# Kernel optimization log

Measured on AMD Instinct MI355X. Metric: run time of the kernel, lower is better.

## Reference

```python
import jax, jax.numpy as jnp
import numpy as np

B, S, D = 1, 2048, 2048      # batch, seq, hidden
E, F, K = 64, 512, 8         # experts, expert ffn dim, top_k


def setup_inputs() -> dict:
    key = jax.random.key(0)
    ks = jax.random.split(key, 7)
    hidden_states = jax.random.normal(ks[0], (B, S, D), jnp.float32)
    gate_w = jax.random.normal(ks[1], (E, D), jnp.float32) * (D ** -0.5)   # router Linear weight
    w_gate = jax.random.normal(ks[2], (E, F, D), jnp.float32) * 0.02       # expert gate_proj
    w_up   = jax.random.normal(ks[3], (E, F, D), jnp.float32) * 0.02       # expert up_proj
    w_down = jax.random.normal(ks[4], (E, D, F), jnp.float32) * 0.02       # expert down_proj
    token_mod  = jax.random.randint(ks[5], (B * S,), -1, 2).astype(jnp.int32)  # {-1,0,1}
    expert_mod = jax.random.randint(ks[6], (E,), -1, 2).astype(jnp.int32)      # {-1,0,1}
    return {"hidden_states": hidden_states, "gate_w": gate_w, "w_gate": w_gate,
            "w_up": w_up, "w_down": w_down, "token_mod": token_mod,
            "expert_mod": expert_mod}


def reference(hidden_states, gate_w, w_gate, w_up, w_down, token_mod, expert_mod):
    bs = B * S
    x = hidden_states.reshape(bs, D)
    # router gate (Linear, no bias): [bs, E]
    logits = x @ gate_w.T
    # modality pre-filtering: mismatch (tok*exp == -1) -> -inf before softmax
    mismatch = (token_mod[:, None] * expert_mod[None, :]) == -1
    logits = jnp.where(mismatch, -jnp.inf, logits)
    probs = jax.nn.softmax(logits, axis=-1)
    rw, sel = jax.lax.top_k(probs, K)                       # [bs,K]
    rw = rw / jnp.sum(rw, axis=-1, keepdims=True)           # renormalize
    # scatter into sparse routing tensor [bs, E]
    sparse = jnp.zeros((bs, E), x.dtype).at[jnp.arange(bs)[:, None], sel].set(rw)
    # expert dispatch (SwiGLU experts), weighted-sum combine
    g = jnp.einsum('td,efd->tef', x, w_gate)                # [bs,E,F]
    u = jnp.einsum('td,efd->tef', x, w_up)
    h = jax.nn.silu(g) * u
    out = jnp.einsum('te,tef,edf->td', sparse, h, w_down)   # [bs,D]
    return out.reshape(B, S, D)
```

## Files before the change

kernel.cpp:

```cpp
#include <hip/hip_runtime.h>
#include <math.h>

#define BS   2048
#define DIM  2048
#define NE   64
#define NF   512
#define TOPK 8

typedef __attribute__((ext_vector_type(8))) short bf16x8;
typedef __attribute__((ext_vector_type(4))) float f32x4;

__device__ __forceinline__ unsigned cvt2(float lo, float hi) {
    unsigned r;
    asm("v_cvt_pk_bf16_f32 %0, %1, %2" : "=v"(r) : "v"(lo), "v"(hi));
    return r;
}
__device__ __forceinline__ unsigned short f2bf(float f) {
    unsigned r = cvt2(f, 0.f);
    return (unsigned short)(r & 0xFFFF);
}

#define SWZ(r, b) (((((r) << 7) + (b)) ^ (((r) & 7) << 4)))

__global__ __launch_bounds__(256) void zero_kernel(float* __restrict__ out, int* __restrict__ count)
{
    const size_t idx = (size_t)blockIdx.x * blockDim.x + threadIdx.x;
    const size_t tot = (size_t)BS * DIM;
    for (size_t i = idx * 4; i < tot; i += (size_t)gridDim.x * blockDim.x * 4) {
        *(float4*)&out[i] = make_float4(0.f, 0.f, 0.f, 0.f);
    }
    if (idx < NE) count[idx] = 0;
}

__global__ __launch_bounds__(256) void router_kernel(
    const float* __restrict__ x, const float* __restrict__ gate_w,
    const int* __restrict__ token_mod, const int* __restrict__ expert_mod,
    int* __restrict__ count, int* __restrict__ list_token, float* __restrict__ list_w)
{
    __shared__ float xs[4 * DIM];
    __shared__ float pr[4][NE];
    const int t0  = blockIdx.x * 4;
    const int tid = threadIdx.x;
    const int lane = tid & 63, wave = tid >> 6;

    float4* xs4 = (float4*)xs;
    const float4* xr = (const float4*)(x + (size_t)t0 * DIM);
    for (int i = tid; i < 4 * (DIM / 4); i += 256) xs4[i] = xr[i];
    __syncthreads();

    for (int j = 0; j < 16; ++j) {
        const int e = wave * 16 + j;
        const float4* gw = (const float4*)(gate_w + (size_t)e * DIM);
        float s0 = 0.f, s1 = 0.f, s2 = 0.f, s3 = 0.f;
        for (int i = lane; i < DIM / 4; i += 64) {
            const float4 g  = gw[i];
            const float4 v0 = xs4[0 * 512 + i];
            const float4 v1 = xs4[1 * 512 + i];
            const float4 v2 = xs4[2 * 512 + i];
            const float4 v3 = xs4[3 * 512 + i];
            s0 += v0.x * g.x + v0.y * g.y + v0.z * g.z + v0.w * g.w;
            s1 += v1.x * g.x + v1.y * g.y + v1.z * g.z + v1.w * g.w;
            s2 += v2.x * g.x + v2.y * g.y + v2.z * g.z + v2.w * g.w;
            s3 += v3.x * g.x + v3.y * g.y + v3.z * g.z + v3.w * g.w;
        }
        #pragma unroll
        for (int off = 32; off > 0; off >>= 1) {
            s0 += __shfl_xor(s0, off, 64);
            s1 += __shfl_xor(s1, off, 64);
            s2 += __shfl_xor(s2, off, 64);
            s3 += __shfl_xor(s3, off, 64);
        }
        if (lane == 0) {
            pr[0][e] = s0; pr[1][e] = s1; pr[2][e] = s2; pr[3][e] = s3;
        }
    }
    __syncthreads();

    {
        const int t  = t0 + wave;
        const int tm = token_mod[t];
        const int em = expert_mod[lane];
        float p = pr[wave][lane];
        if (tm * em == -1) p = -INFINITY;
        float m0 = p;
        #pragma unroll
        for (int off = 32; off > 0; off >>= 1) m0 = fmaxf(m0, __shfl_xor(m0, off, 64));
        p = __expf(p - m0);
        float s8 = 0.f, wsel = 0.f;
        int   esel = 0;
        #pragma unroll
        for (int k = 0; k < TOPK; ++k) {
            float m = p;
            #pragma unroll
            for (int off = 32; off > 0; off >>= 1) m = fmaxf(m, __shfl_xor(m, off, 64));
            const unsigned long long b = __ballot(p == m);
            const int bi = __ffsll((unsigned long long)b) - 1;
            if (lane == bi) p = -1.f;
            if (lane == k) { esel = bi; wsel = m; }
            s8 += m;
        }
        const float inv = 1.f / s8;
        if (lane < TOPK) {
            const int pos = atomicAdd(&count[esel], 1);
            list_token[esel * BS + pos] = t;
            list_w[esel * BS + pos]     = wsel * inv;
        }
    }
}

__global__ void scan_kernel(const int* __restrict__ count, int* __restrict__ offsets)
{
    if (threadIdx.x == 0) {
        int s = 0;
        for (int e = 0; e < NE; ++e) { offsets[e] = s; s += count[e]; }
    }
}

#define GU_BUF 24576
#define GU_X   0
#define GU_G   8192
#define GU_U   16384

#define GU_COMPUTE(BASE)                                                              \
    {                                                                                 \
        _Pragma("unroll")                                                             \
        for (int ks = 0; ks < 2; ++ks) {                                              \
            const int kb = (ks * 32 + (lane >> 4) * 8) * 2;                           \
            bf16x8 a[2], bg[2], bu[2];                                                \
            _Pragma("unroll")                                                         \
            for (int m = 0; m < 2; ++m)                                               \
                a[m] = *(const bf16x8*)&lds[(BASE) + GU_X + SWZ(wr * 32 + m * 16 + (lane & 15), kb)]; \
            _Pragma("unroll")                                                         \
            for (int nn = 0; nn < 2; ++nn) {                                          \
                const int r = wc * 32 + nn * 16 + (lane & 15);                        \
                bg[nn] = *(const bf16x8*)&lds[(BASE) + GU_G + SWZ(r, kb)];            \
                bu[nn] = *(const bf16x8*)&lds[(BASE) + GU_U + SWZ(r, kb)];            \
            }                                                                         \
            _Pragma("unroll")                                                         \
            for (int m = 0; m < 2; ++m)                                               \
                _Pragma("unroll")                                                     \
                for (int nn = 0; nn < 2; ++nn) {                                      \
                    accg[m][nn] = __builtin_amdgcn_mfma_f32_16x16x32_bf16(a[m], bg[nn], accg[m][nn], 0, 0, 0); \
                    accu[m][nn] = __builtin_amdgcn_mfma_f32_16x16x32_bf16(a[m], bu[nn], accu[m][nn], 0, 0, 0); \
                }                                                                     \
        }                                                                             \
    }

__global__ __launch_bounds__(256, 3) void gateup_mfma(
    const float* __restrict__ x,
    const float* __restrict__ w_gate, const float* __restrict__ w_up,
    const int* __restrict__ count, const int* __restrict__ offsets,
    const int* __restrict__ list_token, const float* __restrict__ list_w,
    unsigned short* __restrict__ h)
{
    const int e  = blockIdx.z;
    const int n  = count[e];
    const int m0 = blockIdx.y * 64;
    if (m0 >= n) return;
    const int f0 = blockIdx.x * 64;
    const int mc = min(64, n - m0);

    __shared__ char  lds[2 * GU_BUF];
    __shared__ int   toks[64];
    __shared__ float rws[64];

    const int tid = threadIdx.x;
    if (tid < 64) {
        const int idx = e * BS + m0 + (tid < mc ? tid : 0);
        toks[tid] = list_token[idx];
        rws[tid]  = (tid < mc) ? list_w[idx] : 0.f;
    }
    __syncthreads();

    const int lane = tid & 63, wave = tid >> 6;
    const int wr = wave >> 1, wc = wave & 1;
    const int rr = tid >> 4;
    const int c4 = tid & 15;

    const float* xrow[4];
    #pragma unroll
    for (int i = 0; i < 4; ++i) xrow[i] = x + (size_t)toks[rr + i * 16] * DIM + c4 * 4;
    const float* grow[4];
    const float* urow[4];
    #pragma unroll
    for (int i = 0; i < 4; ++i) {
        grow[i] = w_gate + (size_t)e * NF * DIM + (size_t)(f0 + rr + i * 16) * DIM + c4 * 4;
        urow[i] = w_up   + (size_t)e * NF * DIM + (size_t)(f0 + rr + i * 16) * DIM + c4 * 4;
    }

    f32x4 accg[2][2] = {};
    f32x4 accu[2][2] = {};
    float4 lx[4], lg[4], lu[4];

    #pragma unroll
    for (int i = 0; i < 4; ++i) {
        lx[i] = *(const float4*)(xrow[i]);
        lg[i] = *(const float4*)(grow[i]);
        lu[i] = *(const float4*)(urow[i]);
    }
    #pragma unroll
    for (int i = 0; i < 4; ++i) {
        const int r = rr + i * 16;
        *(uint2*)&lds[GU_X + SWZ(r, c4 * 8)] = make_uint2(cvt2(lx[i].x, lx[i].y), cvt2(lx[i].z, lx[i].w));
        *(uint2*)&lds[GU_G + SWZ(r, c4 * 8)] = make_uint2(cvt2(lg[i].x, lg[i].y), cvt2(lg[i].z, lg[i].w));
        *(uint2*)&lds[GU_U + SWZ(r, c4 * 8)] = make_uint2(cvt2(lu[i].x, lu[i].y), cvt2(lu[i].z, lu[i].w));
    }
    __syncthreads();

    for (int t = 0; t < DIM / 64 - 1; ++t) {
        const int cur = (t & 1) * GU_BUF;
        const int nxt = ((t + 1) & 1) * GU_BUF;
        const int doff = (t + 1) * 64;
        #pragma unroll
        for (int i = 0; i < 4; ++i) {
            lx[i] = *(const float4*)(xrow[i] + doff);
            lg[i] = *(const float4*)(grow[i] + doff);
            lu[i] = *(const float4*)(urow[i] + doff);
        }
        GU_COMPUTE(cur);
        #pragma unroll
        for (int i = 0; i < 4; ++i) {
            const int r = rr + i * 16;
            *(uint2*)&lds[nxt + GU_X + SWZ(r, c4 * 8)] = make_uint2(cvt2(lx[i].x, lx[i].y), cvt2(lx[i].z, lx[i].w));
            *(uint2*)&lds[nxt + GU_G + SWZ(r, c4 * 8)] = make_uint2(cvt2(lg[i].x, lg[i].y), cvt2(lg[i].z, lg[i].w));
            *(uint2*)&lds[nxt + GU_U + SWZ(r, c4 * 8)] = make_uint2(cvt2(lu[i].x, lu[i].y), cvt2(lu[i].z, lu[i].w));
        }
        __syncthreads();
    }
    GU_COMPUTE(((DIM / 64 - 1) & 1) * GU_BUF);

    const int base = offsets[e] + m0;
    #pragma unroll
    for (int m = 0; m < 2; ++m) {
        #pragma unroll
        for (int j = 0; j < 4; ++j) {
            const int tl = wr * 32 + m * 16 + (lane >> 4) * 4 + j;
            if (tl < mc) {
                const float w = rws[tl];
                #pragma unroll
                for (int nn = 0; nn < 2; ++nn) {
                    const int fl = f0 + wc * 32 + nn * 16 + (lane & 15);
                    const float g  = accg[m][nn][j];
                    const float u  = accu[m][nn][j];
                    const float hv = w * u * (g / (1.f + __expf(-g)));
                    h[(size_t)(base + tl) * NF + fl] = f2bf(hv);
                }
            }
        }
    }
}

#define DK_BUF 24576
#define DK_H   0
#define DK_W   8192

#define DK_COMPUTE(BASE)                                                              \
    {                                                                                 \
        _Pragma("unroll")                                                             \
        for (int ks = 0; ks < 2; ++ks) {                                              \
            const int kb = (ks * 32 + (lane >> 4) * 8) * 2;                           \
            bf16x8 a[2], b[4];                                                        \
            _Pragma("unroll")                                                         \
            for (int m = 0; m < 2; ++m)                                               \
                a[m] = *(const bf16x8*)&lds[(BASE) + DK_H + SWZ(wr * 32 + m * 16 + (lane & 15), kb)]; \
            _Pragma("unroll")                                                         \
            for (int nn = 0; nn < 4; ++nn)                                            \
                b[nn] = *(const bf16x8*)&lds[(BASE) + DK_W + SWZ(wc * 64 + nn * 16 + (lane & 15), kb)]; \
            _Pragma("unroll")                                                         \
            for (int m = 0; m < 2; ++m)                                               \
                _Pragma("unroll")                                                     \
                for (int nn = 0; nn < 4; ++nn)                                        \
                    acc[m][nn] = __builtin_amdgcn_mfma_f32_16x16x32_bf16(a[m], b[nn], acc[m][nn], 0, 0, 0); \
        }                                                                             \
    }

__global__ __launch_bounds__(256, 3) void down_mfma(
    const float* __restrict__ w_down,
    const int* __restrict__ count, const int* __restrict__ offsets,
    const int* __restrict__ list_token,
    const unsigned short* __restrict__ h, float* __restrict__ out)
{
    const int e  = blockIdx.z;
    const int n  = count[e];
    const int m0 = blockIdx.y * 64;
    if (m0 >= n) return;
    const int d0 = blockIdx.x * 128;
    const int mc = min(64, n - m0);

    __shared__ char lds[2 * DK_BUF];
    __shared__ int  toks[64];

    const int tid = threadIdx.x;
    if (tid < 64) toks[tid] = list_token[e * BS + m0 + (tid < mc ? tid : 0)];
    __syncthreads();

    const int lane = tid & 63, wave = tid >> 6;
    const int wr = wave >> 1, wc = wave & 1;
    const int rr = tid >> 4;
    const int c4 = tid & 15;
    const int hr = tid >> 3;
    const int hc = (tid & 7) * 8;

    const float* wd  = w_down + (size_t)e * DIM * NF;
    const int   base = offsets[e] + m0;

    const unsigned short* hrow[2];
    #pragma unroll
    for (int i = 0; i < 2; ++i) {
        const int r  = hr + i * 32;
        const int rs = (r < mc ? r : 0);
        hrow[i] = h + (size_t)(base + rs) * NF + hc;
    }
    const float* wrow[8];
    #pragma unroll
    for (int i = 0; i < 8; ++i) wrow[i] = wd + (size_t)(d0 + rr + i * 16) * NF + c4 * 4;

    f32x4 acc[2][4] = {};
    uint4  lh[2];
    float4 lw[8];

    #pragma unroll
    for (int i = 0; i < 2; ++i) lh[i] = *(const uint4*)(hrow[i]);
    #pragma unroll
    for (int i = 0; i < 8; ++i) lw[i] = *(const float4*)(wrow[i]);
    #pragma unroll
    for (int i = 0; i < 2; ++i)
        *(uint4*)&lds[DK_H + SWZ(hr + i * 32, hc * 2)] = lh[i];
    #pragma unroll
    for (int i = 0; i < 8; ++i)
        *(uint2*)&lds[DK_W + SWZ(rr + i * 16, c4 * 8)] = make_uint2(cvt2(lw[i].x, lw[i].y), cvt2(lw[i].z, lw[i].w));
    __syncthreads();

    for (int t = 0; t < NF / 64 - 1; ++t) {
        const int cur = (t & 1) * DK_BUF;
        const int nxt = ((t + 1) & 1) * DK_BUF;
        const int foff = (t + 1) * 64;
        #pragma unroll
        for (int i = 0; i < 2; ++i) lh[i] = *(const uint4*)(hrow[i] + foff);
        #pragma unroll
        for (int i = 0; i < 8; ++i) lw[i] = *(const float4*)(wrow[i] + foff);
        DK_COMPUTE(cur);
        #pragma unroll
        for (int i = 0; i < 2; ++i)
            *(uint4*)&lds[nxt + DK_H + SWZ(hr + i * 32, hc * 2)] = lh[i];
        #pragma unroll
        for (int i = 0; i < 8; ++i)
            *(uint2*)&lds[nxt + DK_W + SWZ(rr + i * 16, c4 * 8)] = make_uint2(cvt2(lw[i].x, lw[i].y), cvt2(lw[i].z, lw[i].w));
        __syncthreads();
    }
    DK_COMPUTE(((NF / 64 - 1) & 1) * DK_BUF);

    #pragma unroll
    for (int m = 0; m < 2; ++m)
        #pragma unroll
        for (int j = 0; j < 4; ++j) {
            const int sl = wr * 32 + m * 16 + (lane >> 4) * 4 + j;
            if (sl < mc) {
                float* orow = out + (size_t)toks[sl] * DIM + d0 + wc * 64 + (lane & 15);
                #pragma unroll
                for (int nn = 0; nn < 4; ++nn)
                    atomicAdd(&orow[nn * 16], acc[m][nn][j]);
            }
        }
}

extern "C" void kernel_launch(void* const* d_in, const int* in_sizes, int n_in,
                              void* d_out, int out_size, void* d_ws, size_t ws_size,
                              hipStream_t stream)
{
    const float* x          = (const float*)d_in[0];
    const float* gate_w     = (const float*)d_in[1];
    const float* w_gate     = (const float*)d_in[2];
    const float* w_up       = (const float*)d_in[3];
    const float* w_down     = (const float*)d_in[4];
    const int*   token_mod  = (const int*)d_in[5];
    const int*   expert_mod = (const int*)d_in[6];
    float* out = (float*)d_out;

    char* ws = (char*)d_ws;
    unsigned short* h  = (unsigned short*)ws;
    int*   count      = (int*)(ws + 16777216);
    int*   offsets    = (int*)(ws + 16777216 + 256);
    int*   list_token = (int*)(ws + 16777216 + 512);
    float* list_w     = (float*)(ws + 16777216 + 512 + (size_t)NE * BS * 4);

    zero_kernel<<<2048, 256, 0, stream>>>(out, count);
    router_kernel<<<BS / 4, 256, 0, stream>>>(x, gate_w, token_mod, expert_mod,
                                              count, list_token, list_w);
    scan_kernel<<<1, 64, 0, stream>>>(count, offsets);

    dim3 g1(NF / 64, BS / 64, NE);
    gateup_mfma<<<g1, 256, 0, stream>>>(x, w_gate, w_up, count, offsets,
                                        list_token, list_w, h);
    dim3 g2(DIM / 128, BS / 64, NE);
    down_mfma<<<g2, 256, 0, stream>>>(w_down, count, offsets, list_token, h, out);
}
```

Measured before the change: 540.1 us.

## Stream fp32 tiles directly to LDS with global_load_lds and convert at fragment load

```diff
diff --git a/kernel.cpp b/kernel.cpp
--- a/kernel.cpp
+++ b/kernel.cpp
@@ -16,11 +16,29 @@
     return r;
 }
 __device__ __forceinline__ unsigned short f2bf(float f) {
-    unsigned r = cvt2(f, 0.f);
-    return (unsigned short)(r & 0xFFFF);
-}
-
-#define SWZ(r, b) (((((r) << 7) + (b)) ^ (((r) & 7) << 4)))
+    return (unsigned short)(cvt2(f, 0.f) & 0xFFFF);
+}
+
+__device__ __forceinline__ void gll16(const void* g, void* l) {
+    __builtin_amdgcn_global_load_lds(
+        (const __attribute__((address_space(1))) void*)g,
+        (__attribute__((address_space(3))) void*)l, 16, 0, 0);
+}
+
+__device__ __forceinline__ bf16x8 fragf32(const char* p, int row, int cb0) {
+    const int sw = row & 7;
+    const f32x4 lo = *(const f32x4*)(p + (row << 7) + ((cb0 ^ sw) << 4));
+    const f32x4 hi = *(const f32x4*)(p + (row << 7) + (((cb0 + 1) ^ sw) << 4));
+    union { bf16x8 v; unsigned u[4]; } r;
+    r.u[0] = cvt2(lo[0], lo[1]);
+    r.u[1] = cvt2(lo[2], lo[3]);
+    r.u[2] = cvt2(hi[0], hi[1]);
+    r.u[3] = cvt2(hi[2], hi[3]);
+    return r.v;
+}
+__device__ __forceinline__ bf16x8 fragbf16(const char* p, int row, int cb) {
+    return *(const bf16x8*)(p + (row << 6) + ((cb ^ ((row >> 1) & 3)) << 4));
+}
 
 __global__ __launch_bounds__(256) void zero_kernel(float* __restrict__ out, int* __restrict__ count)
 {
@@ -116,35 +134,11 @@
     }
 }
 
-#define GU_BUF 24576
-#define GU_X   0
-#define GU_G   8192
-#define GU_U   16384
-
-#define GU_COMPUTE(BASE)                                                              \
-    {                                                                                 \
-        _Pragma("unroll")                                                             \
-        for (int ks = 0; ks < 2; ++ks) {                                              \
-            const int kb = (ks * 32 + (lane >> 4) * 8) * 2;                           \
-            bf16x8 a[2], bg[2], bu[2];                                                \
-            _Pragma("unroll")                                                         \
-            for (int m = 0; m < 2; ++m)                                               \
-                a[m] = *(const bf16x8*)&lds[(BASE) + GU_X + SWZ(wr * 32 + m * 16 + (lane & 15), kb)]; \
-            _Pragma("unroll")                                                         \
-            for (int nn = 0; nn < 2; ++nn) {                                          \
-                const int r = wc * 32 + nn * 16 + (lane & 15);                        \
-                bg[nn] = *(const bf16x8*)&lds[(BASE) + GU_G + SWZ(r, kb)];            \
-                bu[nn] = *(const bf16x8*)&lds[(BASE) + GU_U + SWZ(r, kb)];            \
-            }                                                                         \
-            _Pragma("unroll")                                                         \
-            for (int m = 0; m < 2; ++m)                                               \
-                _Pragma("unroll")                                                     \
-                for (int nn = 0; nn < 2; ++nn) {                                      \
-                    accg[m][nn] = __builtin_amdgcn_mfma_f32_16x16x32_bf16(a[m], bg[nn], accg[m][nn], 0, 0, 0); \
-                    accu[m][nn] = __builtin_amdgcn_mfma_f32_16x16x32_bf16(a[m], bu[nn], accu[m][nn], 0, 0, 0); \
-                }                                                                     \
-        }                                                                             \
-    }
+#define GU_XO 0
+#define GU_GO 8192
+#define GU_UO 16384
+#define GU_STRIDE 24576
+#define GU_NST 64
 
 __global__ __launch_bounds__(256, 3) void gateup_mfma(
     const float* __restrict__ x,
@@ -160,7 +154,7 @@
     const int f0 = blockIdx.x * 64;
     const int mc = min(64, n - m0);
 
-    __shared__ char  lds[2 * GU_BUF];
+    __shared__ char  lds[2 * GU_STRIDE];
     __shared__ int   toks[64];
     __shared__ float rws[64];
 
@@ -174,60 +168,71 @@
 
     const int lane = tid & 63, wave = tid >> 6;
     const int wr = wave >> 1, wc = wave & 1;
-    const int rr = tid >> 4;
-    const int c4 = tid & 15;
-
-    const float* xrow[4];
-    #pragma unroll
-    for (int i = 0; i < 4; ++i) xrow[i] = x + (size_t)toks[rr + i * 16] * DIM + c4 * 4;
-    const float* grow[4];
-    const float* urow[4];
-    #pragma unroll
-    for (int i = 0; i < 4; ++i) {
-        grow[i] = w_gate + (size_t)e * NF * DIM + (size_t)(f0 + rr + i * 16) * DIM + c4 * 4;
-        urow[i] = w_up   + (size_t)e * NF * DIM + (size_t)(f0 + rr + i * 16) * DIM + c4 * 4;
+    const int q  = lane & 7;
+    const int r8 = lane >> 3;
+
+    const float* xsrc[2];
+    const float* gsrc[2];
+    const float* usrc[2];
+    #pragma unroll
+    for (int i = 0; i < 2; ++i) {
+        const int row = wave * 16 + i * 8 + r8;
+        const int cs  = (q ^ (row & 7)) << 2;
+        xsrc[i] = x + (size_t)toks[row] * DIM + cs;
+        gsrc[i] = w_gate + (size_t)e * NF * DIM + (size_t)(f0 + row) * DIM + cs;
+        usrc[i] = w_up   + (size_t)e * NF * DIM + (size_t)(f0 + row) * DIM + cs;
     }
 
     f32x4 accg[2][2] = {};
     f32x4 accu[2][2] = {};
-    float4 lx[4], lg[4], lu[4];
-
-    #pragma unroll
-    for (int i = 0; i < 4; ++i) {
-        lx[i] = *(const float4*)(xrow[i]);
-        lg[i] = *(const float4*)(grow[i]);
-        lu[i] = *(const float4*)(urow[i]);
-    }
-    #pragma unroll
-    for (int i = 0; i < 4; ++i) {
-        const int r = rr + i * 16;
-        *(uint2*)&lds[GU_X + SWZ(r, c4 * 8)] = make_uint2(cvt2(lx[i].x, lx[i].y), cvt2(lx[i].z, lx[i].w));
-        *(uint2*)&lds[GU_G + SWZ(r, c4 * 8)] = make_uint2(cvt2(lg[i].x, lg[i].y), cvt2(lg[i].z, lg[i].w));
-        *(uint2*)&lds[GU_U + SWZ(r, c4 * 8)] = make_uint2(cvt2(lu[i].x, lu[i].y), cvt2(lu[i].z, lu[i].w));
-    }
-    __syncthreads();
-
-    for (int t = 0; t < DIM / 64 - 1; ++t) {
-        const int cur = (t & 1) * GU_BUF;
-        const int nxt = ((t + 1) & 1) * GU_BUF;
-        const int doff = (t + 1) * 64;
-        #pragma unroll
-        for (int i = 0; i < 4; ++i) {
-            lx[i] = *(const float4*)(xrow[i] + doff);
-            lg[i] = *(const float4*)(grow[i] + doff);
-            lu[i] = *(const float4*)(urow[i] + doff);
-        }
-        GU_COMPUTE(cur);
-        #pragma unroll
-        for (int i = 0; i < 4; ++i) {
-            const int r = rr + i * 16;
-            *(uint2*)&lds[nxt + GU_X + SWZ(r, c4 * 8)] = make_uint2(cvt2(lx[i].x, lx[i].y), cvt2(lx[i].z, lx[i].w));
-            *(uint2*)&lds[nxt + GU_G + SWZ(r, c4 * 8)] = make_uint2(cvt2(lg[i].x, lg[i].y), cvt2(lg[i].z, lg[i].w));
-            *(uint2*)&lds[nxt + GU_U + SWZ(r, c4 * 8)] = make_uint2(cvt2(lu[i].x, lu[i].y), cvt2(lu[i].z, lu[i].w));
-        }
-        __syncthreads();
-    }
-    GU_COMPUTE(((DIM / 64 - 1) & 1) * GU_BUF);
+    const int cb0 = (lane >> 4) * 2;
+    const int ldd = wave * 2048;
+
+    #pragma unroll
+    for (int i = 0; i < 2; ++i) {
+        gll16(xsrc[i], &lds[GU_XO + ldd + i * 1024]);
+        gll16(gsrc[i], &lds[GU_GO + ldd + i * 1024]);
+        gll16(usrc[i], &lds[GU_UO + ldd + i * 1024]);
+    }
+
+    for (int t = 0; t < GU_NST; ++t) {
+        const char* buf = &lds[(t & 1) * GU_STRIDE];
+        if (t + 1 < GU_NST) {
+            const int nb = ((t + 1) & 1) * GU_STRIDE;
+            const int ko = (t + 1) * 32;
+            #pragma unroll
+            for (int i = 0; i < 2; ++i) {
+                gll16(xsrc[i] + ko, &lds[nb + GU_XO + ldd + i * 1024]);
+                gll16(gsrc[i] + ko, &lds[nb + GU_GO + ldd + i * 1024]);
+                gll16(usrc[i] + ko, &lds[nb + GU_UO + ldd + i * 1024]);
+            }
+            asm volatile("s_waitcnt vmcnt(6)" ::: "memory");
+        } else {
+            asm volatile("s_waitcnt vmcnt(0)" ::: "memory");
+        }
+        __builtin_amdgcn_s_barrier();
+        __builtin_amdgcn_sched_barrier(0);
+
+        bf16x8 a[2], bg[2], bu[2];
+        #pragma unroll
+        for (int m = 0; m < 2; ++m)
+            a[m] = fragf32(buf + GU_XO, wr * 32 + m * 16 + (lane & 15), cb0);
+        #pragma unroll
+        for (int nn = 0; nn < 2; ++nn) {
+            const int r = wc * 32 + nn * 16 + (lane & 15);
+            bg[nn] = fragf32(buf + GU_GO, r, cb0);
+            bu[nn] = fragf32(buf + GU_UO, r, cb0);
+        }
+        #pragma unroll
+        for (int m = 0; m < 2; ++m)
+            #pragma unroll
+            for (int nn = 0; nn < 2; ++nn) {
+                accg[m][nn] = __builtin_amdgcn_mfma_f32_16x16x32_bf16(a[m], bg[nn], accg[m][nn], 0, 0, 0);
+                accu[m][nn] = __builtin_amdgcn_mfma_f32_16x16x32_bf16(a[m], bu[nn], accu[m][nn], 0, 0, 0);
+            }
+        __builtin_amdgcn_sched_barrier(0);
+        __builtin_amdgcn_s_barrier();
+    }
 
     const int base = offsets[e] + m0;
     #pragma unroll
@@ -250,29 +255,10 @@
     }
 }
 
-#define DK_BUF 24576
-#define DK_H   0
-#define DK_W   8192
-
-#define DK_COMPUTE(BASE)                                                              \
-    {                                                                                 \
-        _Pragma("unroll")                                                             \
-        for (int ks = 0; ks < 2; ++ks) {                                              \
-            const int kb = (ks * 32 + (lane >> 4) * 8) * 2;                           \
-            bf16x8 a[2], b[4];                                                        \
-            _Pragma("unroll")                                                         \
-            for (int m = 0; m < 2; ++m)                                               \
-                a[m] = *(const bf16x8*)&lds[(BASE) + DK_H + SWZ(wr * 32 + m * 16 + (lane & 15), kb)]; \
-            _Pragma("unroll")                                                         \
-            for (int nn = 0; nn < 4; ++nn)                                            \
-                b[nn] = *(const bf16x8*)&lds[(BASE) + DK_W + SWZ(wc * 64 + nn * 16 + (lane & 15), kb)]; \
-            _Pragma("unroll")                                                         \
-            for (int m = 0; m < 2; ++m)                                               \
-                _Pragma("unroll")                                                     \
-                for (int nn = 0; nn < 4; ++nn)                                        \
-                    acc[m][nn] = __builtin_amdgcn_mfma_f32_16x16x32_bf16(a[m], b[nn], acc[m][nn], 0, 0, 0); \
-        }                                                                             \
-    }
+#define DK_HO 0
+#define DK_WO 4096
+#define DK_STRIDE 20480
+#define DK_NST 16
 
 __global__ __launch_bounds__(256, 3) void down_mfma(
     const float* __restrict__ w_down,
@@ -287,7 +273,7 @@
     const int d0 = blockIdx.x * 128;
     const int mc = min(64, n - m0);
 
-    __shared__ char lds[2 * DK_BUF];
+    __shared__ char lds[2 * DK_STRIDE];
     __shared__ int  toks[64];
 
     const int tid = threadIdx.x;
@@ -296,59 +282,62 @@
 
     const int lane = tid & 63, wave = tid >> 6;
     const int wr = wave >> 1, wc = wave & 1;
-    const int rr = tid >> 4;
-    const int c4 = tid & 15;
-    const int hr = tid >> 3;
-    const int hc = (tid & 7) * 8;
+    const int q  = lane & 7,  r8 = lane >> 3;
+    const int q4 = lane & 3,  r4 = lane >> 2;
 
     const float* wd  = w_down + (size_t)e * DIM * NF;
     const int   base = offsets[e] + m0;
 
-    const unsigned short* hrow[2];
-    #pragma unroll
-    for (int i = 0; i < 2; ++i) {
-        const int r  = hr + i * 32;
-        const int rs = (r < mc ? r : 0);
-        hrow[i] = h + (size_t)(base + rs) * NF + hc;
-    }
-    const float* wrow[8];
-    #pragma unroll
-    for (int i = 0; i < 8; ++i) wrow[i] = wd + (size_t)(d0 + rr + i * 16) * NF + c4 * 4;
+    const int hrow = wave * 16 + r4;
+    const unsigned short* hsrc =
+        h + (size_t)(base + (hrow < mc ? hrow : 0)) * NF + ((q4 ^ ((hrow >> 1) & 3)) << 3);
+    const float* wsrc[4];
+    #pragma unroll
+    for (int i = 0; i < 4; ++i) {
+        const int row = wave * 32 + i * 8 + r8;
+        wsrc[i] = wd + (size_t)(d0 + row) * NF + ((q ^ (row & 7)) << 2);
+    }
 
     f32x4 acc[2][4] = {};
-    uint4  lh[2];
-    float4 lw[8];
-
-    #pragma unroll
-    for (int i = 0; i < 2; ++i) lh[i] = *(const uint4*)(hrow[i]);
-    #pragma unroll
-    for (int i = 0; i < 8; ++i) lw[i] = *(const float4*)(wrow[i]);
-    #pragma unroll
-    for (int i = 0; i < 2; ++i)
-        *(uint4*)&lds[DK_H + SWZ(hr + i * 32, hc * 2)] = lh[i];
-    #pragma unroll
-    for (int i = 0; i < 8; ++i)
-        *(uint2*)&lds[DK_W + SWZ(rr + i * 16, c4 * 8)] = make_uint2(cvt2(lw[i].x, lw[i].y), cvt2(lw[i].z, lw[i].w));
-    __syncthreads();
-
-    for (int t = 0; t < NF / 64 - 1; ++t) {
-        const int cur = (t & 1) * DK_BUF;
-        const int nxt = ((t + 1) & 1) * DK_BUF;
-        const int foff = (t + 1) * 64;
-        #pragma unroll
-        for (int i = 0; i < 2; ++i) lh[i] = *(const uint4*)(hrow[i] + foff);
-        #pragma unroll
-        for (int i = 0; i < 8; ++i) lw[i] = *(const float4*)(wrow[i] + foff);
-        DK_COMPUTE(cur);
-        #pragma unroll
-        for (int i = 0; i < 2; ++i)
-            *(uint4*)&lds[nxt + DK_H + SWZ(hr + i * 32, hc * 2)] = lh[i];
-        #pragma unroll
-        for (int i = 0; i < 8; ++i)
-            *(uint2*)&lds[nxt + DK_W + SWZ(rr + i * 16, c4 * 8)] = make_uint2(cvt2(lw[i].x, lw[i].y), cvt2(lw[i].z, lw[i].w));
-        __syncthreads();
-    }
-    DK_COMPUTE(((NF / 64 - 1) & 1) * DK_BUF);
+    const int cb0 = (lane >> 4) * 2;
+    const int cbh = lane >> 4;
+
+    gll16(hsrc, &lds[DK_HO + wave * 1024]);
+    #pragma unroll
+    for (int i = 0; i < 4; ++i)
+        gll16(wsrc[i], &lds[DK_WO + wave * 4096 + i * 1024]);
+
+    for (int t = 0; t < DK_NST; ++t) {
+        const char* buf = &lds[(t & 1) * DK_STRIDE];
+        if (t + 1 < DK_NST) {
+            const int nb = ((t + 1) & 1) * DK_STRIDE;
+            const int fo = (t + 1) * 32;
+            gll16(hsrc + fo, &lds[nb + DK_HO + wave * 1024]);
+            #pragma unroll
+            for (int i = 0; i < 4; ++i)
+                gll16(wsrc[i] + fo, &lds[nb + DK_WO + wave * 4096 + i * 1024]);
+            asm volatile("s_waitcnt vmcnt(5)" ::: "memory");
+        } else {
+            asm volatile("s_waitcnt vmcnt(0)" ::: "memory");
+        }
+        __builtin_amdgcn_s_barrier();
+        __builtin_amdgcn_sched_barrier(0);
+
+        bf16x8 a[2], b[4];
+        #pragma unroll
+        for (int m = 0; m < 2; ++m)
+            a[m] = fragbf16(buf + DK_HO, wr * 32 + m * 16 + (lane & 15), cbh);
+        #pragma unroll
+        for (int nn = 0; nn < 4; ++nn)
+            b[nn] = fragf32(buf + DK_WO, wc * 64 + nn * 16 + (lane & 15), cb0);
+        #pragma unroll
+        for (int m = 0; m < 2; ++m)
+            #pragma unroll
+            for (int nn = 0; nn < 4; ++nn)
+                acc[m][nn] = __builtin_amdgcn_mfma_f32_16x16x32_bf16(a[m], b[nn], acc[m][nn], 0, 0, 0);
+        __builtin_amdgcn_sched_barrier(0);
+        __builtin_amdgcn_s_barrier();
+    }
 
     #pragma unroll
     for (int m = 0; m < 2; ++m)
```

New measurement: 574.5 us. +6.4%, slower.
